# Kernel tuning notes

Hardware: AMD Instinct MI355X
Metric: run time of the kernel (lower is better)

Reference implementation:

```python
import jax, jax.numpy as jnp
import numpy as np

D_MODEL = 1024
N_HEADS = 16
D_HEAD = D_MODEL // N_HEADS


def setup_inputs() -> dict:
    key = jax.random.key(0)
    ks = jax.random.split(key, 5)
    scale = 1.0 / np.sqrt(D_MODEL)
    return {
        "x": jax.random.normal(ks[0], (2, 2048, D_MODEL), dtype=jnp.float32),
        "W_q": jax.random.normal(ks[1], (D_MODEL, D_MODEL), dtype=jnp.float32) * scale,
        "W_k": jax.random.normal(ks[2], (D_MODEL, D_MODEL), dtype=jnp.float32) * scale,
        "W_v": jax.random.normal(ks[3], (D_MODEL, D_MODEL), dtype=jnp.float32) * scale,
        "W_o": jax.random.normal(ks[4], (D_MODEL, D_MODEL), dtype=jnp.float32) * scale,
    }


def reference(x, W_q, W_k, W_v, W_o):
    B, S, _ = x.shape
    # nn.Linear computes x @ W.T; weights stored [out, in]
    def proj(W):
        y = jnp.einsum("bsd,ed->bse", x, W)
        return y.reshape(B, S, N_HEADS, D_HEAD).transpose(0, 2, 1, 3)  # [B,H,S,Dh]

    q, k, v = proj(W_q), proj(W_k), proj(W_v)
    scores = jnp.einsum("bhqd,bhkd->bhqk", q, k) / jnp.sqrt(jnp.float32(D_HEAD))
    causal = jnp.triu(jnp.ones((S, S), dtype=bool), k=1)
    scores = jnp.where(causal, -jnp.inf, scores)
    attn = jax.nn.softmax(scores, axis=-1)
    out = jnp.einsum("bhqk,bhkd->bhqd", attn, v)  # [B,H,S,Dh]
    out = out.transpose(0, 2, 1, 3).reshape(B, S, D_MODEL)
    return jnp.einsum("bsd,ed->bse", out, W_o)
```

## Files before the change

kernel.cpp:

```cpp
#include <hip/hip_runtime.h>


#define DMODEL 1024
#define NHEADS 16
#define DHEAD  64
#define SEQ    2048
#define BATCH  2
#define MROWS  (BATCH * SEQ)

typedef __bf16 bf16x8 __attribute__((ext_vector_type(8)));
typedef __bf16 bf16x4 __attribute__((ext_vector_type(4)));
typedef float  f32x4  __attribute__((ext_vector_type(4)));

__device__ __forceinline__ f32x4 mfma16(bf16x8 a, bf16x8 b, f32x4 c) {
    return __builtin_amdgcn_mfma_f32_16x16x32_bf16(a, b, c, 0, 0, 0);
}

__device__ __forceinline__ bf16x8 ld8(const float* p) {
    const f32x4 a0 = *(const f32x4*)p;
    const f32x4 a1 = *(const f32x4*)(p + 4);
    bf16x8 v;
    v[0] = (__bf16)a0[0]; v[1] = (__bf16)a0[1];
    v[2] = (__bf16)a0[2]; v[3] = (__bf16)a0[3];
    v[4] = (__bf16)a1[0]; v[5] = (__bf16)a1[1];
    v[6] = (__bf16)a1[2]; v[7] = (__bf16)a1[3];
    return v;
}

__device__ __forceinline__ void gll16(const __bf16* g, __bf16* l) {
    __builtin_amdgcn_global_load_lds(
        (const __attribute__((address_space(1))) void*)g,
        (__attribute__((address_space(3))) void*)l,
        16, 0, 0);
}

__global__ __launch_bounds__(256) void cvt_kernel(const float* __restrict__ x,
                                                  const float* __restrict__ Wq,
                                                  const float* __restrict__ Wk,
                                                  const float* __restrict__ Wv,
                                                  const float* __restrict__ Wo,
                                                  __bf16* __restrict__ xb,
                                                  __bf16* __restrict__ wcat) {
    const int c = blockIdx.x * 256 + threadIdx.x;
    if (c < 524288) {
        *(bf16x8*)(xb + (size_t)c * 8) = ld8(x + (size_t)c * 8);
    } else {
        const int i = c - 524288;
        const int w = i >> 17;
        const int j = i & 131071;
        const float* src = (w == 0) ? Wq : (w == 1) ? Wk : (w == 2) ? Wv : Wo;
        *(bf16x8*)(wcat + (size_t)w * DMODEL * DMODEL + (size_t)j * 8) =
            ld8(src + (size_t)j * 8);
    }
}

template <typename TC, int MI>
__device__ __forceinline__ void gemm_bb_body(const __bf16* __restrict__ A,
                                             const __bf16* __restrict__ W,
                                             TC* __restrict__ C,
                                             __bf16* __restrict__ VT,
                                             bool vt, int m0, int bn0, int cn0,
                                             float scale) {
    constexpr int K = DMODEL;
    constexpr int TM = MI * 32;
    __shared__ __align__(16) __bf16 As[TM][64];
    __shared__ __align__(16) __bf16 Bs[128][64];

    const int tid  = threadIdx.x;
    const int lane = tid & 63;
    const int wave = tid >> 6;
    const int quad = lane >> 4;
    const int l16  = lane & 15;
    const int wm   = wave & 1;
    const int wn   = wave >> 1;

    const int sr8 = lane >> 3;
    const int scs = ((lane & 7) ^ sr8) * 8;

    const int g8 = l16 & 7;

    f32x4 acc[MI][4] = {};

    for (int k0 = 0; k0 < K; k0 += 64) {
        __syncthreads();
#pragma unroll
        for (int j = 0; j < MI; ++j) {
            const int row = wave * (MI * 8) + j * 8;
            gll16(A + (size_t)(m0 + row + sr8) * K + k0 + scs, &As[row][0]);
        }
#pragma unroll
        for (int j = 0; j < 4; ++j) {
            const int row = wave * 32 + j * 8;
            gll16(W + (size_t)(bn0 + row + sr8) * K + k0 + scs, &Bs[row][0]);
        }
        __syncthreads();

#pragma unroll
        for (int h = 0; h < 2; ++h) {
            bf16x8 af[MI], bfr[4];
#pragma unroll
            for (int i = 0; i < MI; ++i)
                af[i] = *(const bf16x8*)(
                    &As[wm * (MI * 16) + i * 16 + l16][((h * 4 + quad) ^ g8) * 8]);
#pragma unroll
            for (int j = 0; j < 4; ++j)
                bfr[j] = *(const bf16x8*)(
                    &Bs[wn * 64 + j * 16 + l16][((h * 4 + quad) ^ g8) * 8]);
#pragma unroll
            for (int mi = 0; mi < MI; ++mi)
#pragma unroll
                for (int ni = 0; ni < 4; ++ni)
                    acc[mi][ni] = mfma16(af[mi], bfr[ni], acc[mi][ni]);
        }
    }

    if (!vt) {
#pragma unroll
        for (int mi = 0; mi < MI; ++mi)
#pragma unroll
            for (int ni = 0; ni < 4; ++ni)
#pragma unroll
                for (int r = 0; r < 4; ++r) {
                    int row = m0 + wm * (MI * 16) + mi * 16 + quad * 4 + r;
                    int col = cn0 + wn * 64 + ni * 16 + l16;
                    C[(size_t)row * DMODEL + col] = (TC)(acc[mi][ni][r] * scale);
                }
    } else {
#pragma unroll
        for (int mi = 0; mi < MI; ++mi)
#pragma unroll
            for (int ni = 0; ni < 4; ++ni) {
                const int m  = m0 + wm * (MI * 16) + mi * 16 + quad * 4;
                const int hd = cn0 + wn * 64 + ni * 16 + l16;
                bf16x4 v4;
#pragma unroll
                for (int r = 0; r < 4; ++r) v4[r] = (__bf16)acc[mi][ni][r];
                *(bf16x4*)(VT + (size_t)hd * MROWS + m) = v4;
            }
    }
}

#define QSCALE 0.1803368801111204f

__global__ __launch_bounds__(256) void qkv_kernel(const __bf16* __restrict__ X,
                                                  const __bf16* __restrict__ wcat,
                                                  __bf16* __restrict__ Q,
                                                  __bf16* __restrict__ K,
                                                  __bf16* __restrict__ VT) {
    const int bn0 = blockIdx.x * 128;
    const int z   = bn0 >> 10;
    const int cn0 = bn0 - (z << 10);
    __bf16* Y = (z == 0) ? Q : K;
    const float scale = (z == 0) ? QSCALE : 1.0f;
    gemm_bb_body<__bf16, 4>(X, wcat, Y, VT, z == 2,
                            blockIdx.y * 128, bn0, cn0, scale);
}

__global__ __launch_bounds__(256) void out_gemm_kernel(const __bf16* __restrict__ A,
                                                       const __bf16* __restrict__ W,
                                                       float* __restrict__ C) {
    gemm_bb_body<float, 2>(A, W, C, nullptr, false,
                           blockIdx.y * 64, blockIdx.x * 128, blockIdx.x * 128,
                           1.0f);
}

__global__ __launch_bounds__(256) void attn_kernel(const __bf16* __restrict__ Q,
                                                   const __bf16* __restrict__ Kg,
                                                   const __bf16* __restrict__ VTg,
                                                   __bf16* __restrict__ O) {
    const int bh  = blockIdx.x;
    const int y   = blockIdx.y;
    const int ya  = y >> 3, yr = y & 7;
    const int qt2 = (ya == 0) ? (31 - yr)
                  : (ya == 1) ? (16 + yr)
                  : (ya == 2) ? (15 - yr)
                  :             yr;
    const int b = bh >> 4, h = bh & 15;
    const size_t base = (size_t)b * SEQ * DMODEL + (size_t)h * DHEAD;

    const int tid  = threadIdx.x;
    const int lane = tid & 63;
    const int wave = tid >> 6;
    const int quad = lane >> 4;
    const int l16  = lane & 15;

    __shared__ __align__(16) __bf16 Ks[64][64];
    __shared__ __align__(16) __bf16 Vs[64][64];
    __shared__ __align__(16) __bf16 Ps[4][2][16][40];

    const int sr = lane >> 3;
    const int sc = ((lane & 7) ^ sr) * 8;

    const int qrow = qt2 * 64 + wave * 16 + l16;

    const bf16x8 qf0 = *(const bf16x8*)(Q + base + (size_t)qrow * DMODEL + quad * 8);
    const bf16x8 qf1 = *(const bf16x8*)(Q + base + (size_t)qrow * DMODEL + 32 + quad * 8);

    const __bf16* kp = Kg + base + (size_t)(wave * 16 + sr) * DMODEL + sc;
    const __bf16* vp = VTg + (size_t)(h * 64 + wave * 16 + sr) * MROWS
                           + (size_t)b * SEQ + sc;

    bf16x8 ones;
#pragma unroll
    for (int i = 0; i < 8; ++i) ones[i] = (__bf16)1.0f;

    f32x4 oacc[4] = {};
    f32x4 lacc = {};

    const int ntiles = qt2 + 1;
    const int gsw = (l16 & 7);

    for (int kt = 0; kt < ntiles; ++kt) {
        const int k0 = kt * 64;
        __syncthreads();
        {
            const __bf16* kpt = kp + (size_t)k0 * DMODEL;
            const __bf16* vpt = vp + k0;
            gll16(kpt, &Ks[wave * 16][0]);
            gll16(kpt + (size_t)8 * DMODEL, &Ks[wave * 16 + 8][0]);
            gll16(vpt, &Vs[wave * 16][0]);
            gll16(vpt + (size_t)8 * MROWS, &Vs[wave * 16 + 8][0]);
        }
        __syncthreads();

        const bool diag = (kt == ntiles - 1);

        f32x4 s[4];
#pragma unroll
        for (int g = 0; g < 4; ++g) {
            const bf16x8 kfa = *(const bf16x8*)(&Ks[g * 16 + l16][(quad ^ gsw) * 8]);
            const bf16x8 kfb = *(const bf16x8*)(&Ks[g * 16 + l16][((quad + 4) ^ gsw) * 8]);
            f32x4 t = {};
            t = mfma16(kfa, qf0, t);
            t = mfma16(kfb, qf1, t);
            s[g] = t;
        }

        bf16x4 w4[4];
        if (!diag) {
#pragma unroll
            for (int g = 0; g < 4; ++g)
#pragma unroll
                for (int r = 0; r < 4; ++r)
                    w4[g][r] = (__bf16)exp2f(s[g][r]);
        } else {
#pragma unroll
            for (int g = 0; g < 4; ++g)
#pragma unroll
                for (int r = 0; r < 4; ++r) {
                    const int kk = k0 + g * 16 + quad * 4 + r;
                    w4[g][r] = (kk <= qrow) ? (__bf16)exp2f(s[g][r]) : (__bf16)0.f;
                }
        }

#pragma unroll
        for (int g = 0; g < 4; ++g)
            *(bf16x4*)(&Ps[wave][g >> 1][l16][(g & 1) * 16 + quad * 4]) = w4[g];

        const bf16x8 pf0 = *(const bf16x8*)(&Ps[wave][0][l16][quad * 8]);
        const bf16x8 pf1 = *(const bf16x8*)(&Ps[wave][1][l16][quad * 8]);
        lacc = mfma16(ones, pf0, lacc);
        lacc = mfma16(ones, pf1, lacc);
#pragma unroll
        for (int f = 0; f < 4; ++f) {
            const bf16x8 vfa = *(const bf16x8*)(&Vs[f * 16 + l16][(quad ^ gsw) * 8]);
            const bf16x8 vfb = *(const bf16x8*)(&Vs[f * 16 + l16][((quad + 4) ^ gsw) * 8]);
            f32x4 t = oacc[f];
            t = mfma16(vfa, pf0, t);
            t = mfma16(vfb, pf1, t);
            oacc[f] = t;
        }
    }

    const float l_i = lacc[0];
    const float inv = (l_i > 0.f) ? (1.f / l_i) : 0.f;
#pragma unroll
    for (int f = 0; f < 4; ++f) {
        bf16x4 o;
#pragma unroll
        for (int r = 0; r < 4; ++r) o[r] = (__bf16)(oacc[f][r] * inv);
        *(bf16x4*)(O + base + (size_t)qrow * DMODEL + f * 16 + quad * 4) = o;
    }
}

extern "C" void kernel_launch(void* const* d_in, const int* in_sizes, int n_in,
                              void* d_out, int out_size, void* d_ws, size_t ws_size,
                              hipStream_t stream) {
    const float* x  = (const float*)d_in[0];
    const float* Wq = (const float*)d_in[1];
    const float* Wk = (const float*)d_in[2];
    const float* Wv = (const float*)d_in[3];
    const float* Wo = (const float*)d_in[4];
    float* out = (float*)d_out;

    const size_t tm = (size_t)MROWS * DMODEL;
    const size_t tw = (size_t)DMODEL * DMODEL;
    __bf16* Q    = (__bf16*)d_ws;
    __bf16* K    = Q + tm;
    __bf16* VT   = K + tm;
    __bf16* xb   = VT + tm;
    __bf16* wcat = xb + tm;

    cvt_kernel<<<4096, 256, 0, stream>>>(x, Wq, Wk, Wv, Wo, xb, wcat);

    dim3 g1(3072 / 128, MROWS / 128);
    qkv_kernel<<<g1, 256, 0, stream>>>(xb, wcat, Q, K, VT);

    dim3 g2(BATCH * NHEADS, SEQ / 64);
    attn_kernel<<<g2, 256, 0, stream>>>(Q, K, VT, Q);

    dim3 g3(DMODEL / 128, MROWS / 64);
    out_gemm_kernel<<<g3, 256, 0, stream>>>(Q, wcat + 3 * tw, out);
}
```

Before: 180.8 us.

## Double-buffer GEMM shared-memory tiles with K-step of 32

Restructures the projection GEMM main loop to use two shared-memory buffers with a K-tile of 32 instead of a single 64-wide buffer. The next tile's global-to-LDS load is issued before computing on the current one, which overlaps loading with MFMA work and needs only one barrier per iteration. The XOR swizzle is dropped in favour of plain row-major 32-wide rows, which may bring back LDS bank conflicts, and the smaller K step doubles the iteration count and the number of barriers. Each wave now loads 16 rows per buffer half, which assumes MI is 2 or 4.

```diff
diff --git a/kernel.cpp b/kernel.cpp
--- a/kernel.cpp
+++ b/kernel.cpp
@@ -63,8 +63,8 @@
                                              float scale) {
     constexpr int K = DMODEL;
     constexpr int TM = MI * 32;
-    __shared__ __align__(16) __bf16 As[TM][64];
-    __shared__ __align__(16) __bf16 Bs[128][64];
+    __shared__ __align__(16) __bf16 As[2][TM][32];
+    __shared__ __align__(16) __bf16 Bs[2][128][32];
 
     const int tid  = threadIdx.x;
     const int lane = tid & 63;
@@ -74,44 +74,47 @@
     const int wm   = wave & 1;
     const int wn   = wave >> 1;
 
-    const int sr8 = lane >> 3;
-    const int scs = ((lane & 7) ^ sr8) * 8;
-
-    const int g8 = l16 & 7;
+    const int srow = lane >> 2;
+    const int scol = (lane & 3) * 8;
+
+    const __bf16* a0p = A + (size_t)(m0 + wave * 16 + srow) * K + scol;
+    const __bf16* a1p = A + (size_t)(m0 + 64 + wave * 16 + srow) * K + scol;
+    const __bf16* b0p = W + (size_t)(bn0 + wave * 16 + srow) * K + scol;
+    const __bf16* b1p = W + (size_t)(bn0 + 64 + wave * 16 + srow) * K + scol;
 
     f32x4 acc[MI][4] = {};
 
-    for (int k0 = 0; k0 < K; k0 += 64) {
+    gll16(a0p, &As[0][wave * 16][0]);
+    if (MI == 4) gll16(a1p, &As[0][64 + wave * 16][0]);
+    gll16(b0p, &Bs[0][wave * 16][0]);
+    gll16(b1p, &Bs[0][64 + wave * 16][0]);
+    __syncthreads();
+
+    int cur = 0;
+    for (int k0 = 0; k0 < K; k0 += 32) {
+        if (k0 + 32 < K) {
+            const int kn = k0 + 32;
+            gll16(a0p + kn, &As[cur ^ 1][wave * 16][0]);
+            if (MI == 4) gll16(a1p + kn, &As[cur ^ 1][64 + wave * 16][0]);
+            gll16(b0p + kn, &Bs[cur ^ 1][wave * 16][0]);
+            gll16(b1p + kn, &Bs[cur ^ 1][64 + wave * 16][0]);
+        }
+
+        bf16x8 af[MI], bfr[4];
+#pragma unroll
+        for (int i = 0; i < MI; ++i)
+            af[i] = *(const bf16x8*)(&As[cur][wm * (MI * 16) + i * 16 + l16][quad * 8]);
+#pragma unroll
+        for (int j = 0; j < 4; ++j)
+            bfr[j] = *(const bf16x8*)(&Bs[cur][wn * 64 + j * 16 + l16][quad * 8]);
+#pragma unroll
+        for (int mi = 0; mi < MI; ++mi)
+#pragma unroll
+            for (int ni = 0; ni < 4; ++ni)
+                acc[mi][ni] = mfma16(af[mi], bfr[ni], acc[mi][ni]);
+
         __syncthreads();
-#pragma unroll
-        for (int j = 0; j < MI; ++j) {
-            const int row = wave * (MI * 8) + j * 8;
-            gll16(A + (size_t)(m0 + row + sr8) * K + k0 + scs, &As[row][0]);
-        }
-#pragma unroll
-        for (int j = 0; j < 4; ++j) {
-            const int row = wave * 32 + j * 8;
-            gll16(W + (size_t)(bn0 + row + sr8) * K + k0 + scs, &Bs[row][0]);
-        }
-        __syncthreads();
-
-#pragma unroll
-        for (int h = 0; h < 2; ++h) {
-            bf16x8 af[MI], bfr[4];
-#pragma unroll
-            for (int i = 0; i < MI; ++i)
-                af[i] = *(const bf16x8*)(
-                    &As[wm * (MI * 16) + i * 16 + l16][((h * 4 + quad) ^ g8) * 8]);
-#pragma unroll
-            for (int j = 0; j < 4; ++j)
-                bfr[j] = *(const bf16x8*)(
-                    &Bs[wn * 64 + j * 16 + l16][((h * 4 + quad) ^ g8) * 8]);
-#pragma unroll
-            for (int mi = 0; mi < MI; ++mi)
-#pragma unroll
-                for (int ni = 0; ni < 4; ++ni)
-                    acc[mi][ni] = mfma16(af[mi], bfr[ni], acc[mi][ni]);
-        }
+        cur ^= 1;
     }
 
     if (!vt) {
```

New measurement: 181.2 us. About the same (+0.2%).
